# Kernel tuning notes

Hardware: AMD Instinct MI355X
Metric: run time of the kernel (lower is better)

## Reference

```python
import jax, jax.numpy as jnp
import numpy as np

L, D, H, F, E, K = 2, 512, 8, 2048, 8, 2
V, B, S, T, PAD = 32000, 2, 1024, 1024, 0


def _pe(n, d):
    pos = jnp.arange(n, dtype=jnp.float32)[:, None]
    div = jnp.exp(jnp.arange(0, d, 2, dtype=jnp.float32) * (-np.log(10000.0) / d))
    pe = jnp.zeros((n, d), jnp.float32)
    pe = pe.at[:, 0::2].set(jnp.sin(pos * div)).at[:, 1::2].set(jnp.cos(pos * div))
    return pe


def _ln(x, g, b):
    m = x.mean(-1, keepdims=True)
    v = ((x - m) ** 2).mean(-1, keepdims=True)
    return (x - m) / jnp.sqrt(v + 1e-5) * g + b


def _mha(q_in, k_in, v_in, w, b, mask):
    # w: [4,D,D] (q,k,v,out), b: [4,D]; mask broadcastable to [B,H,Sq,Sk] (True=keep)
    Bq, Sq, Dm = q_in.shape
    Sk = k_in.shape[1]
    dk = Dm // H
    q = (q_in @ w[0] + b[0]).reshape(Bq, Sq, H, dk).transpose(0, 2, 1, 3)
    k = (k_in @ w[1] + b[1]).reshape(Bq, Sk, H, dk).transpose(0, 2, 1, 3)
    v = (v_in @ w[2] + b[2]).reshape(Bq, Sk, H, dk).transpose(0, 2, 1, 3)
    s = jnp.einsum('bhqd,bhkd->bhqk', q, k) / np.sqrt(dk).astype(np.float32)
    s = jnp.where(mask, s, jnp.float32(-1e9))
    a = jax.nn.softmax(s, axis=-1)
    c = jnp.einsum('bhqk,bhkd->bhqd', a, v).transpose(0, 2, 1, 3).reshape(Bq, Sq, Dm)
    return c @ w[3] + b[3]


def _moe(x, gw, gb, w1, b1, w2, b2):
    # token-choice top-k routing with softmax gate probs (no renormalization)
    Bx, Sx, Dm = x.shape
    N = Bx * Sx
    xf = x.reshape(N, Dm)
    probs = jax.nn.softmax(xf @ gw + gb, axis=-1)              # [N,E]
    topv, topi = jax.lax.top_k(probs, K)                        # [N,K]
    comb = jnp.zeros_like(probs).at[jnp.arange(N)[:, None], topi].set(topv)  # [N,E] sparse combine weights
    h = jax.nn.relu(jnp.einsum('nd,edf->nef', xf, w1) + b1)     # [N,E,F]
    eo = jnp.einsum('nef,efd->ned', h, w2) + b2                 # [N,E,D]
    y = jnp.einsum('ne,ned->nd', comb, eo)
    return y.reshape(Bx, Sx, Dm)


def setup_inputs():
    key = jax.random.key(0)
    ks = iter(jax.random.split(key, 32))
    sd, sf = 1.0 / np.sqrt(D), 1.0 / np.sqrt(F)

    def nrm(shape, scale):
        return jax.random.normal(next(ks), shape, jnp.float32) * np.float32(scale)

    inp = {}
    inp['src'] = jax.random.randint(next(ks), (B, S), 0, V)
    inp['tgt'] = jax.random.randint(next(ks), (B, T), 0, V)
    inp['enc_emb'] = nrm((V, D), 0.02).at[PAD].set(0.0)
    inp['dec_emb'] = nrm((V, D), 0.02).at[PAD].set(0.0)
    inp['enc_attn_w'] = nrm((L, 4, D, D), sd)
    inp['enc_attn_b'] = jnp.zeros((L, 4, D), jnp.float32)
    inp['enc_ln_g'] = jnp.ones((L, 2, D), jnp.float32)
    inp['enc_ln_b'] = jnp.zeros((L, 2, D), jnp.float32)
    inp['enc_gate_w'] = nrm((L, D, E), sd)
    inp['enc_gate_b'] = jnp.zeros((L, E), jnp.float32)
    inp['enc_w1'] = nrm((L, E, D, F), sd)
    inp['enc_b1'] = jnp.zeros((L, E, F), jnp.float32)
    inp['enc_w2'] = nrm((L, E, F, D), sf)
    inp['enc_b2'] = jnp.zeros((L, E, D), jnp.float32)
    inp['dec_sa_w'] = nrm((L, 4, D, D), sd)
    inp['dec_sa_b'] = jnp.zeros((L, 4, D), jnp.float32)
    inp['dec_ca_w'] = nrm((L, 4, D, D), sd)
    inp['dec_ca_b'] = jnp.zeros((L, 4, D), jnp.float32)
    inp['dec_ln_g'] = jnp.ones((L, 3, D), jnp.float32)
    inp['dec_ln_b'] = jnp.zeros((L, 3, D), jnp.float32)
    inp['dec_gate_w'] = nrm((L, D, E), sd)
    inp['dec_gate_b'] = jnp.zeros((L, E), jnp.float32)
    inp['dec_w1'] = nrm((L, E, D, F), sd)
    inp['dec_b1'] = jnp.zeros((L, E, F), jnp.float32)
    inp['dec_w2'] = nrm((L, E, F, D), sf)
    inp['dec_b2'] = jnp.zeros((L, E, D), jnp.float32)
    inp['out_w'] = nrm((D, V), sd)
    inp['out_b'] = jnp.zeros((V,), jnp.float32)
    return inp


def reference(src, tgt, enc_emb, dec_emb, enc_attn_w, enc_attn_b, enc_ln_g, enc_ln_b,
              enc_gate_w, enc_gate_b, enc_w1, enc_b1, enc_w2, enc_b2,
              dec_sa_w, dec_sa_b, dec_ca_w, dec_ca_b, dec_ln_g, dec_ln_b,
              dec_gate_w, dec_gate_b, dec_w1, dec_b1, dec_w2, dec_b2, out_w, out_b):
    src_mask = (src != PAD)[:, None, None, :]                                  # [B,1,1,S]
    causal = jnp.tril(jnp.ones((T, T), bool))
    tgt_mask = (tgt != PAD)[:, None, None, :] & causal[None, None]             # [B,1,T,T]

    x = enc_emb[src] + _pe(S, D)[None]                                         # dropout = identity (eval)
    for l in range(L):
        a = _mha(x, x, x, enc_attn_w[l], enc_attn_b[l], src_mask)
        x = _ln(x + a, enc_ln_g[l, 0], enc_ln_b[l, 0])
        f = _moe(x, enc_gate_w[l], enc_gate_b[l], enc_w1[l], enc_b1[l], enc_w2[l], enc_b2[l])
        x = _ln(x + f, enc_ln_g[l, 1], enc_ln_b[l, 1])
    enc_out = x

    y = dec_emb[tgt] + _pe(T, D)[None]
    for l in range(L):
        a = _mha(y, y, y, dec_sa_w[l], dec_sa_b[l], tgt_mask)
        y = _ln(y + a, dec_ln_g[l, 0], dec_ln_b[l, 0])
        c = _mha(y, enc_out, enc_out, dec_ca_w[l], dec_ca_b[l], src_mask)
        y = _ln(y + c, dec_ln_g[l, 1], dec_ln_b[l, 1])
        f = _moe(y, dec_gate_w[l], dec_gate_b[l], dec_w1[l], dec_b1[l], dec_w2[l], dec_b2[l])
        y = _ln(y + f, dec_ln_g[l, 2], dec_ln_b[l, 2])

    return y @ out_w + out_b                                                    # [B,T,V]
```

## Files before the change

### kernel.cpp

```cpp
#include <hip/hip_runtime.h>
#include <hip/hip_bf16.h>

#define L_ 2
#define D_ 512
#define H_ 8
#define DK_ 64
#define F_ 2048
#define E_ 8
#define V_ 32000
#define B_ 2
#define S_ 1024
#define T_ 1024
#define NTOK (B_*S_)
#define MAXPAD 5120
#define RBLK   40
#define QLD 1536

typedef unsigned short u16;
typedef _Float16 f16x8 __attribute__((ext_vector_type(8)));
typedef _Float16 f16x4 __attribute__((ext_vector_type(4)));
typedef float f32x4 __attribute__((ext_vector_type(4)));

__device__ __forceinline__ void gload16(const void* g, const void* l) {
    __builtin_amdgcn_global_load_lds(
        (const __attribute__((address_space(1))) void*)g,
        (__attribute__((address_space(3))) void*)l, 16, 0, 0);
}

__device__ __forceinline__ void split_f16(float v, _Float16& h, _Float16& l) {
    h = (_Float16)v;
    l = (_Float16)(v - (float)h);
}

__global__ __launch_bounds__(256) void embed_pe(const int* __restrict__ toks,
                                                const float* __restrict__ emb,
                                                _Float16* __restrict__ oh,
                                                _Float16* __restrict__ ol, int Slen)
{
    int n = blockIdx.x;
    int spos = n % Slen;
    int tok = toks[n];
    const float* erow = emb + (size_t)tok * D_;
    size_t rb = (size_t)n * D_;
    for (int j = threadIdx.x; j < D_; j += 256) {
        int i = j >> 1;
        float arg = (float)spos * expf(-(float)i * 0.035977892f);
        float pe = (j & 1) ? cosf(arg) : sinf(arg);
        float v = erow[j] + pe;
        _Float16 h, l; split_f16(v, h, l);
        oh[rb + j] = h; ol[rb + j] = l;
    }
}

template<bool WLO>
__global__ __launch_bounds__(256) void transpose_w(const float* __restrict__ in,
                                                   _Float16* __restrict__ oh,
                                                   _Float16* __restrict__ ol, int R, int C)
{
    __shared__ float t[64][65];
    size_t sb = (size_t)blockIdx.z * R * C;
    in += sb; oh += sb; if (WLO) ol += sb;
    int c0 = blockIdx.x * 64, r0 = blockIdx.y * 64;
    int tid = threadIdx.x;
    {
        int r = tid >> 4;
        int cq = (tid & 15) * 4;
        #pragma unroll
        for (int p = 0; p < 4; ++p) {
            int rr = r + p * 16;
            float4 v = *(const float4*)&in[(size_t)(r0 + rr) * C + c0 + cq];
            t[rr][cq] = v.x; t[rr][cq + 1] = v.y; t[rr][cq + 2] = v.z; t[rr][cq + 3] = v.w;
        }
    }
    __syncthreads();
    int rp = (tid & 15) * 4;
    int cb = tid >> 4;
    #pragma unroll
    for (int p = 0; p < 4; ++p) {
        int c = cb + p * 16;
        f16x4 hv, lv;
        #pragma unroll
        for (int j = 0; j < 4; ++j) {
            float v = t[rp + j][c];
            _Float16 h = (_Float16)v;
            hv[j] = h;
            if (WLO) lv[j] = (_Float16)(v - (float)h);
        }
        *(f16x4*)&oh[(size_t)(c0 + c) * R + r0 + rp] = hv;
        if (WLO) *(f16x4*)&ol[(size_t)(c0 + c) * R + r0 + rp] = lv;
    }
}

__global__ __launch_bounds__(256) void transpose_w3(
    const float* __restrict__ i0, _Float16* __restrict__ h0, _Float16* __restrict__ l0,
    const float* __restrict__ i1, _Float16* __restrict__ h1, _Float16* __restrict__ l1,
    const float* __restrict__ i2, _Float16* __restrict__ h2, _Float16* __restrict__ l2)
{
    __shared__ float t[64][65];
    int set = blockIdx.z >> 3, sub = blockIdx.z & 7;
    const float* in = (set == 0) ? i0 : (set == 1) ? i1 : i2;
    _Float16* oh = (set == 0) ? h0 : (set == 1) ? h1 : h2;
    _Float16* ol = (set == 0) ? l0 : (set == 1) ? l1 : l2;
    size_t sb = (size_t)sub * D_ * D_;
    in += sb; oh += sb; ol += sb;
    int c0 = blockIdx.x * 64, r0 = blockIdx.y * 64;
    int tid = threadIdx.x;
    {
        int r = tid >> 4;
        int cq = (tid & 15) * 4;
        #pragma unroll
        for (int p = 0; p < 4; ++p) {
            int rr = r + p * 16;
            float4 v = *(const float4*)&in[(size_t)(r0 + rr) * D_ + c0 + cq];
            t[rr][cq] = v.x; t[rr][cq + 1] = v.y; t[rr][cq + 2] = v.z; t[rr][cq + 3] = v.w;
        }
    }
    __syncthreads();
    int rp = (tid & 15) * 4;
    int cb = tid >> 4;
    #pragma unroll
    for (int p = 0; p < 4; ++p) {
        int c = cb + p * 16;
        f16x4 hv, lv;
        #pragma unroll
        for (int j = 0; j < 4; ++j) {
            float v = t[rp + j][c];
            _Float16 h = (_Float16)v;
            hv[j] = h;
            lv[j] = (_Float16)(v - (float)h);
        }
        *(f16x4*)&oh[(size_t)(c0 + c) * D_ + r0 + rp] = hv;
        *(f16x4*)&ol[(size_t)(c0 + c) * D_ + r0 + rp] = lv;
    }
}

template<int MODE, bool RELU, int OUTMODE, int PASSES, int TM, int TN, bool SWZ>
__global__ __launch_bounds__(256, 2) void gemm_mfma(
    const _Float16* __restrict__ Ah, const _Float16* __restrict__ Al,
    const _Float16* __restrict__ Wh, const _Float16* __restrict__ Wl,
    const float* __restrict__ biasbase,
    float* __restrict__ Cf, _Float16* __restrict__ Ch, _Float16* __restrict__ Cl,
    _Float16* __restrict__ vt_h, _Float16* __restrict__ vt_l, int cbase,
    int M, int Kd, int N, int ldc,
    const int* __restrict__ route_tok, const int* __restrict__ rb_expert,
    const int* __restrict__ pad_base, const int* __restrict__ counts)
{
    constexpr int AR = TM / 32;
    constexpr int BR = TN / 32;
    int bx = blockIdx.x, by = blockIdx.y;
    if (SWZ) {
        int total = gridDim.x * gridDim.y;
        int n = by * gridDim.x + bx;
        int q = total >> 3;
        int w2 = (n & 7) * q + (n >> 3);
        bx = w2 % gridDim.x; by = w2 / gridDim.x;
    }
    int row0 = bx * TM;
    const _Float16* Wmh = Wh;
    const _Float16* Wml = Wl;
    const float* bias = biasbase;
    int vend = M;
    if (MODE != 0) {
        int total = pad_base[E_];
        if (row0 >= total) return;
        int e = rb_expert[row0 >> 7];
        vend = pad_base[e] + counts[e];
        Wmh = Wh + (size_t)e * Kd * N;
        if (PASSES == 3) Wml = Wl + (size_t)e * Kd * N;
        bias = biasbase + (size_t)e * N;
    }
    int col0 = by * TN;
    int tid = threadIdx.x;
    int lane = tid & 63, w = tid >> 6;
    int wm = w >> 1, wn = w & 1;

    __shared__ _Float16 lds[(PASSES == 3 ? 2 : 1) * (TM + TN) * 64];
    _Float16* lAh = lds;
    _Float16* lBh = lds + TM * 64;
    _Float16* lAl = (PASSES == 3) ? lds + (TM + TN) * 64 : nullptr;
    _Float16* lBl = (PASSES == 3) ? lds + (TM + TN) * 64 + TM * 64 : nullptr;

    int srow8 = lane >> 3;
    int q8 = lane & 7;
    size_t aoff[AR], boff[BR];
    #pragma unroll
    for (int j = 0; j < AR; ++j) {
        int m = w * (TM / 4) + j * 8 + srow8;
        int gr = row0 + m;
        int ar = (MODE == 1) ? route_tok[gr] : gr;
        int ss = (q8 ^ (m & 7)) << 3;
        aoff[j] = (size_t)ar * Kd + ss;
    }
    #pragma unroll
    for (int j = 0; j < BR; ++j) {
        int m = w * (TN / 4) + j * 8 + srow8;
        int ss = (q8 ^ (m & 7)) << 3;
        boff[j] = (size_t)(col0 + m) * Kd + ss;
    }

    f32x4 zero4 = {0.f, 0.f, 0.f, 0.f};
    f32x4 acc[AR][BR];
    #pragma unroll
    for (int i = 0; i < AR; ++i)
        #pragma unroll
        for (int j = 0; j < BR; ++j) acc[i][j] = zero4;

    int lm = lane & 15, kg = lane >> 4;

    for (int k0 = 0; k0 < Kd; k0 += 64) {
        #pragma unroll
        for (int j = 0; j < AR; ++j) {
            int lb = (w * (TM / 4) + j * 8) * 64;
            gload16(Ah + aoff[j] + k0, lAh + lb);
            if (PASSES == 3) gload16(Al + aoff[j] + k0, lAl + lb);
        }
        #pragma unroll
        for (int j = 0; j < BR; ++j) {
            int lb = (w * (TN / 4) + j * 8) * 64;
            gload16(Wmh + boff[j] + k0, lBh + lb);
            if (PASSES == 3) gload16(Wml + boff[j] + k0, lBl + lb);
        }
        __syncthreads();
        #pragma unroll
        for (int ks = 0; ks < 2; ++ks) {
            f16x8 ah[AR], bh[BR];
            #pragma unroll
            for (int i = 0; i < AR; ++i) {
                int m = wm * (TM / 2) + i * 16 + lm;
                ah[i] = *(const f16x8*)&lAh[m * 64 + ((((ks << 2) + kg) ^ (m & 7)) << 3)];
            }
            #pragma unroll
            for (int j = 0; j < BR; ++j) {
                int n = wn * (TN / 2) + j * 16 + lm;
                bh[j] = *(const f16x8*)&lBh[n * 64 + ((((ks << 2) + kg) ^ (n & 7)) << 3)];
            }
            #pragma unroll
            for (int i = 0; i < AR; ++i)
                #pragma unroll
                for (int jn = 0; jn < BR; ++jn)
                    acc[i][jn] = __builtin_amdgcn_mfma_f32_16x16x32_f16(ah[i], bh[jn], acc[i][jn], 0, 0, 0);
            if (PASSES == 3) {
                f16x8 bl[BR];
                #pragma unroll
                for (int j = 0; j < BR; ++j) {
                    int n = wn * (TN / 2) + j * 16 + lm;
                    bl[j] = *(const f16x8*)&lBl[n * 64 + ((((ks << 2) + kg) ^ (n & 7)) << 3)];
                }
                #pragma unroll
                for (int i = 0; i < AR; ++i)
                    #pragma unroll
                    for (int jn = 0; jn < BR; ++jn)
                        acc[i][jn] = __builtin_amdgcn_mfma_f32_16x16x32_f16(ah[i], bl[jn], acc[i][jn], 0, 0, 0);
                f16x8 al[AR];
                #pragma unroll
// ... 190 lines not shown
                    pv[jn][r] = p;
                    psum += p;
                }
                psum += __shfl_xor(psum, 1);
                psum += __shfl_xor(psum, 2);
                psum += __shfl_xor(psum, 4);
                psum += __shfl_xor(psum, 8);
                lreg[r] += psum;
                mreg[r] = mnew;
            }

            #pragma unroll
            for (int jn = 0; jn < 4; ++jn) {
                int col = jn * 16 + lm;
                #pragma unroll
                for (int r = 0; r < 4; ++r) {
                    int rr = (lane >> 4) * 4 + r;
                    int idx = rr * 64 + (((col >> 3) ^ (rr & 7)) << 3) + (col & 7);
                    _Float16 hh, ll; split_f16(pv[jn][r], hh, ll);
                    lPh[idx] = hh; lPl[idx] = ll;
                }
            }

            #pragma unroll
            for (int ks = 0; ks < 2; ++ks) {
                int poff = lm * 64 + ((((ks << 2) + kg) ^ (lm & 7)) << 3);
                f16x8 pah = *(const f16x8*)&lPh[poff];
                f16x8 pal = *(const f16x8*)&lPl[poff];
                #pragma unroll
                for (int jn = 0; jn < 4; ++jn) {
                    int n = jn * 16 + lm;
                    int noff = n * 64 + ((((ks << 2) + kg) ^ (n & 7)) << 3);
                    f16x8 vbh = *(const f16x8*)&lVh[noff];
                    f16x8 vbl = *(const f16x8*)&lVl[noff];
                    od[jn] = __builtin_amdgcn_mfma_f32_16x16x32_f16(pah, vbh, od[jn], 0, 0, 0);
                    od[jn] = __builtin_amdgcn_mfma_f32_16x16x32_f16(pah, vbl, od[jn], 0, 0, 0);
                    od[jn] = __builtin_amdgcn_mfma_f32_16x16x32_f16(pal, vbh, od[jn], 0, 0, 0);
                }
            }
        }
        __syncthreads();
    }

    float* mrg = (float*)(smem + 32768);
    if (kh == 1) {
        float* mp = mrg + ((size_t)qg * 64 + lane) * 24;
        #pragma unroll
        for (int jn = 0; jn < 4; ++jn)
            #pragma unroll
            for (int r = 0; r < 4; ++r) mp[jn * 4 + r] = od[jn][r];
        #pragma unroll
        for (int r = 0; r < 4; ++r) { mp[16 + r] = mreg[r]; mp[20 + r] = lreg[r]; }
    }
    __syncthreads();
    if (kh == 0) {
        float* mp = mrg + ((size_t)qg * 64 + lane) * 24;
        #pragma unroll
        for (int r = 0; r < 4; ++r) {
            float m1 = mp[16 + r], l1 = mp[20 + r];
            float m = fmaxf(mreg[r], m1);
            float c0 = expf(mreg[r] - m), c1 = expf(m1 - m);
            float inv = 1.0f / (lreg[r] * c0 + l1 * c1);
            size_t rbase = (size_t)(tb + qrow[r]) * D_ + h * DK_;
            #pragma unroll
            for (int jn = 0; jn < 4; ++jn) {
                float o = (od[jn][r] * c0 + mp[jn * 4 + r] * c1) * inv;
                _Float16 hh, ll; split_f16(o, hh, ll);
                int d = jn * 16 + lm;
                ch[rbase + d] = hh; cl[rbase + d] = ll;
            }
        }
    }
}

template<bool GATE>
__global__ __launch_bounds__(256) void ln_add(const _Float16* __restrict__ xh,
                                              const _Float16* __restrict__ xl,
                                              const float* __restrict__ r,
                                              const float* __restrict__ g,
                                              const float* __restrict__ be,
                                              _Float16* __restrict__ oh,
                                              _Float16* __restrict__ ol,
                                              const float* __restrict__ gw,
                                              const float* __restrict__ gb,
                                              float* __restrict__ lg)
{
    int row = blockIdx.x;
    size_t rb = (size_t)row * D_;
    int tid = threadIdx.x;
    float v0 = (float)xh[rb + tid] + (float)xl[rb + tid] + r[rb + tid];
    float v1 = (float)xh[rb + tid + 256] + (float)xl[rb + tid + 256] + r[rb + tid + 256];
    float s = v0 + v1;
    for (int off = 32; off; off >>= 1) s += __shfl_down(s, off);
    __shared__ float red[8];
    __shared__ float gred[4][E_];
    int lane = tid & 63, wid = tid >> 6;
    if (!lane) red[wid] = s;
    __syncthreads();
    if (!tid) red[4] = (red[0] + red[1] + red[2] + red[3]) * (1.0f / 512.0f);
    __syncthreads();
    float m = red[4];
    float d0 = v0 - m, d1 = v1 - m;
    s = d0 * d0 + d1 * d1;
    for (int off = 32; off; off >>= 1) s += __shfl_down(s, off);
    if (!lane) red[wid] = s;
    __syncthreads();
    if (!tid) red[5] = rsqrtf((red[0] + red[1] + red[2] + red[3]) * (1.0f / 512.0f) + 1e-5f);
    __syncthreads();
    float rstd = red[5];
    float y0 = d0 * rstd * g[tid] + be[tid];
    float y1 = d1 * rstd * g[tid + 256] + be[tid + 256];
    _Float16 h, l;
    split_f16(y0, h, l); oh[rb + tid] = h; ol[rb + tid] = l;
    split_f16(y1, h, l); oh[rb + tid + 256] = h; ol[rb + tid + 256] = l;
    if (GATE) {
        float acc[E_];
        const float* g0 = gw + (size_t)tid * E_;
        const float* g1 = gw + (size_t)(tid + 256) * E_;
        #pragma unroll
        for (int e = 0; e < E_; ++e) acc[e] = y0 * g0[e] + y1 * g1[e];
        #pragma unroll
        for (int e = 0; e < E_; ++e)
            for (int off = 32; off; off >>= 1) acc[e] += __shfl_down(acc[e], off);
        if (!lane) {
            #pragma unroll
            for (int e = 0; e < E_; ++e) gred[wid][e] = acc[e];
        }
        __syncthreads();
        if (tid < E_)
            lg[(size_t)row * E_ + tid] = gred[0][tid] + gred[1][tid] + gred[2][tid] + gred[3][tid] + gb[tid];
    }
}

__global__ __launch_bounds__(256) void ln_add_moe(const _Float16* __restrict__ xh,
                                                  const _Float16* __restrict__ xl,
                                                  const float* __restrict__ eo,
                                                  const float* __restrict__ topv,
                                                  const int* __restrict__ route_row,
                                                  const float* __restrict__ g,
                                                  const float* __restrict__ be,
                                                  _Float16* __restrict__ oh,
                                                  _Float16* __restrict__ ol)
{
    int row = blockIdx.x;
    int r0 = route_row[row * 2], r1 = route_row[row * 2 + 1];
    float w0 = topv[row * 2], w1 = topv[row * 2 + 1];
    size_t rb = (size_t)row * D_;
    const float* e0 = eo + (size_t)r0 * D_;
    const float* e1 = eo + (size_t)r1 * D_;
    int tid = threadIdx.x;
    float v0 = (float)xh[rb + tid] + (float)xl[rb + tid] + w0 * e0[tid] + w1 * e1[tid];
    float v1 = (float)xh[rb + tid + 256] + (float)xl[rb + tid + 256] + w0 * e0[tid + 256] + w1 * e1[tid + 256];
    float s = v0 + v1;
    for (int off = 32; off; off >>= 1) s += __shfl_down(s, off);
    __shared__ float red[8];
    int lane = tid & 63, wid = tid >> 6;
    if (!lane) red[wid] = s;
    __syncthreads();
    if (!tid) red[4] = (red[0] + red[1] + red[2] + red[3]) * (1.0f / 512.0f);
    __syncthreads();
    float m = red[4];
    float d0 = v0 - m, d1 = v1 - m;
    s = d0 * d0 + d1 * d1;
    for (int off = 32; off; off >>= 1) s += __shfl_down(s, off);
    if (!lane) red[wid] = s;
    __syncthreads();
    if (!tid) red[5] = rsqrtf((red[0] + red[1] + red[2] + red[3]) * (1.0f / 512.0f) + 1e-5f);
    __syncthreads();
    float rstd = red[5];
    float y0 = d0 * rstd * g[tid] + be[tid];
    float y1 = d1 * rstd * g[tid + 256] + be[tid + 256];
    _Float16 h, l;
    split_f16(y0, h, l); oh[rb + tid] = h; ol[rb + tid] = l;
    split_f16(y1, h, l); oh[rb + tid + 256] = h; ol[rb + tid + 256] = l;
}

__global__ __launch_bounds__(1024) void gate_top2_routes(const float* __restrict__ lg,
                                                         float* __restrict__ topv,
                                                         int* __restrict__ route_tok,
                                                         int* __restrict__ route_row,
                                                         int* __restrict__ counts,
                                                         int* __restrict__ pad_base,
                                                         int* __restrict__ rb_expert)
{
    __shared__ int eid[NTOK * 2];
    __shared__ unsigned short chist[256][8];
    __shared__ unsigned short segb[8][16];
    __shared__ int pb[E_ + 1];
    __shared__ int cnt[E_];
    int t = threadIdx.x;
    #pragma unroll
    for (int s2 = 0; s2 < 2; ++s2) {
        int n = t * 2 + s2;
        float l0[E_], p[E_];
        float m = -1e30f;
        #pragma unroll
        for (int e = 0; e < E_; ++e) { l0[e] = lg[n * E_ + e]; m = fmaxf(m, l0[e]); }
        float su = 0.f;
        #pragma unroll
        for (int e = 0; e < E_; ++e) { p[e] = expf(l0[e] - m); su += p[e]; }
        float inv = 1.0f / su;
        int i1 = 0; float v1 = p[0];
        #pragma unroll
        for (int e = 1; e < E_; ++e) if (p[e] > v1) { v1 = p[e]; i1 = e; }
        int i2 = -1; float v2 = -1.f;
        #pragma unroll
        for (int e = 0; e < E_; ++e) if (e != i1 && p[e] > v2) { v2 = p[e]; i2 = e; }
        topv[n * 2] = v1 * inv; topv[n * 2 + 1] = v2 * inv;
        eid[n * 2] = i1; eid[n * 2 + 1] = i2;
    }
    #pragma unroll
    for (int g = 0; g < 5; ++g) route_tok[t + 1024 * g] = 0;
    __syncthreads();

    if (t < 256) {
        int r[16];
        #pragma unroll
        for (int i = 0; i < 16; ++i) r[i] = eid[t * 16 + i];
        #pragma unroll
        for (int e = 0; e < 8; ++e) {
            int h = 0;
            #pragma unroll
            for (int i = 0; i < 16; ++i) h += (r[i] == e) ? 1 : 0;
            chist[t][e] = (unsigned short)h;
        }
    }
    __syncthreads();

    if (t < 128) {
        int e = t >> 4, seg = t & 15;
        int s = 0;
        #pragma unroll
        for (int i = 0; i < 16; ++i) s += chist[seg * 16 + i][e];
        segb[e][seg] = (unsigned short)s;
    }
    __syncthreads();
    if (t < 8) {
        int run = 0;
        #pragma unroll
        for (int sg = 0; sg < 16; ++sg) {
            int v = segb[t][sg];
            segb[t][sg] = (unsigned short)run;
            run += v;
        }
        cnt[t] = run;
        counts[t] = run;
    }
    __syncthreads();
    if (t < 128) {
        int e = t >> 4, seg = t & 15;
        int run = segb[e][seg];
        #pragma unroll
        for (int i = 0; i < 16; ++i) {
            int c = seg * 16 + i;
            int v = chist[c][e];
            chist[c][e] = (unsigned short)run;
            run += v;
        }
    }
    __syncthreads();

    if (t == 0) {
        int pad = 0;
        for (int e = 0; e < 8; ++e) {
            pb[e] = pad;
            pad_base[e] = pad;
            int nb = (cnt[e] + 127) >> 7;
            for (int rb = 0; rb < nb; ++rb) rb_expert[(pad >> 7) + rb] = e;
            pad += nb << 7;
        }
        pb[8] = pad;
        pad_base[8] = pad;
    }
    __syncthreads();

    if (t < 256) {
        int r[16];
        #pragma unroll
        for (int i = 0; i < 16; ++i) r[i] = eid[t * 16 + i];
        #pragma unroll
        for (int e = 0; e < 8; ++e) {
            int o = pb[e] + chist[t][e];
            #pragma unroll
            for (int i = 0; i < 16; ++i) {
                if (r[i] == e) {
                    int slot = t * 16 + i;
                    route_tok[o] = slot >> 1;
                    route_row[slot] = o;
                    o++;
                }
            }
        }
    }
}

extern "C" void kernel_launch(void* const* d_in, const int* in_sizes, int n_in,
                              void* d_out, int out_size, void* d_ws, size_t ws_size,
                              hipStream_t stream)
{
    const int*   src        = (const int*)  d_in[0];
    const int*   tgt        = (const int*)  d_in[1];
    const float* enc_emb    = (const float*)d_in[2];
    const float* dec_emb    = (const float*)d_in[3];
    const float* enc_attn_w = (const float*)d_in[4];
    const float* enc_attn_b = (const float*)d_in[5];
    const float* enc_ln_g   = (const float*)d_in[6];
    const float* enc_ln_b   = (const float*)d_in[7];
    const float* enc_gate_w = (const float*)d_in[8];
    const float* enc_gate_b = (const float*)d_in[9];
    const float* enc_w1     = (const float*)d_in[10];
    const float* enc_b1     = (const float*)d_in[11];
    const float* enc_w2     = (const float*)d_in[12];
    const float* enc_b2     = (const float*)d_in[13];
    const float* dec_sa_w   = (const float*)d_in[14];
    const float* dec_sa_b   = (const float*)d_in[15];
    const float* dec_ca_w   = (const float*)d_in[16];
    const float* dec_ca_b   = (const float*)d_in[17];
    const float* dec_ln_g   = (const float*)d_in[18];
    const float* dec_ln_b   = (const float*)d_in[19];
    const float* dec_gate_w = (const float*)d_in[20];
    const float* dec_gate_b = (const float*)d_in[21];
    const float* dec_w1     = (const float*)d_in[22];
    const float* dec_b1     = (const float*)d_in[23];
    const float* dec_w2     = (const float*)d_in[24];
    const float* dec_b2     = (const float*)d_in[25];
    const float* out_w      = (const float*)d_in[26];
    const float* out_b      = (const float*)d_in[27];
    float* out = (float*)d_out;

    char* ob = (char*)d_out;
    size_t oc = 0;
    auto dalloc = [&](size_t bytes) { char* p = ob + oc; oc += (bytes + 255) & ~(size_t)255; return p; };
    _Float16* qkv_h  = (_Float16*)dalloc((size_t)NTOK * QLD * 2);
    _Float16* qkv_l  = (_Float16*)dalloc((size_t)NTOK * QLD * 2);
    _Float16* vt_h   = (_Float16*)dalloc((size_t)16 * 64 * 1024 * 2);
    _Float16* vt_l   = (_Float16*)dalloc((size_t)16 * 64 * 1024 * 2);
    float* aout  = (float*)dalloc((size_t)NTOK * D_ * 4);
    _Float16* ctx_h = (_Float16*)dalloc((size_t)NTOK * D_ * 2);
    _Float16* ctx_l = (_Float16*)dalloc((size_t)NTOK * D_ * 2);
    _Float16* encA_h = (_Float16*)dalloc((size_t)L_ * 4 * D_ * D_ * 2);
    _Float16* encA_l = (_Float16*)dalloc((size_t)L_ * 4 * D_ * D_ * 2);
    _Float16* saA_h  = (_Float16*)dalloc((size_t)L_ * 4 * D_ * D_ * 2);
    _Float16* saA_l  = (_Float16*)dalloc((size_t)L_ * 4 * D_ * D_ * 2);
    _Float16* caA_h  = (_Float16*)dalloc((size_t)L_ * 4 * D_ * D_ * 2);
    _Float16* caA_l  = (_Float16*)dalloc((size_t)L_ * 4 * D_ * D_ * 2);
    _Float16* xA_h = (_Float16*)dalloc((size_t)NTOK * D_ * 2);
    _Float16* xA_l = (_Float16*)dalloc((size_t)NTOK * D_ * 2);
    _Float16* xB_h = (_Float16*)dalloc((size_t)NTOK * D_ * 2);
    _Float16* xB_l = (_Float16*)dalloc((size_t)NTOK * D_ * 2);
    _Float16* yA_h = (_Float16*)dalloc((size_t)NTOK * D_ * 2);
    _Float16* yA_l = (_Float16*)dalloc((size_t)NTOK * D_ * 2);
    _Float16* yB_h = (_Float16*)dalloc((size_t)NTOK * D_ * 2);
    _Float16* yB_l = (_Float16*)dalloc((size_t)NTOK * D_ * 2);

    char* wp = (char*)d_ws;
    size_t wc = 0;
    auto walloc = [&](size_t bytes) { char* p = wp + wc; wc += (bytes + 255) & ~(size_t)255; return p; };
    _Float16* outwT_h = (_Float16*)walloc((size_t)V_ * D_ * 2);
    _Float16* final_h = (_Float16*)walloc((size_t)NTOK * D_ * 2);
    size_t wsz = (size_t)L_ * E_ * D_ * F_;
    _Float16* ew1t_h = (_Float16*)walloc(wsz * 2);
    _Float16* ew1t_l = (_Float16*)walloc(wsz * 2);
    _Float16* ew2t_h = (_Float16*)walloc(wsz * 2);
    _Float16* ew2t_l = (_Float16*)walloc(wsz * 2);
    _Float16* dw1t_h = (_Float16*)walloc(wsz * 2);
    _Float16* dw1t_l = (_Float16*)walloc(wsz * 2);
    _Float16* dw2t_h = (_Float16*)walloc(wsz * 2);
    _Float16* dw2t_l = (_Float16*)walloc(wsz * 2);
    _Float16* hbuf_h  = (_Float16*)walloc((size_t)MAXPAD * F_ * 2);
    _Float16* hbuf_l  = (_Float16*)walloc((size_t)MAXPAD * F_ * 2);
    float*    eobuf   = (float*)walloc((size_t)MAXPAD * D_ * 4);
    float* lg   = (float*)walloc((size_t)NTOK * E_ * 4);
    float* topv = (float*)walloc((size_t)NTOK * 2 * 4);
    int*   route_tok = (int*)walloc((size_t)MAXPAD * 4);
    int*   route_row = (int*)walloc((size_t)NTOK * 2 * 4);
    int*   counts    = (int*)walloc(64);
    int*   pad_base  = (int*)walloc(64);
    int*   rb_expert = (int*)walloc((size_t)128 * 4);

    transpose_w3<<<dim3(8, 8, 24), 256, 0, stream>>>(
        enc_attn_w, encA_h, encA_l, dec_sa_w, saA_h, saA_l, dec_ca_w, caA_h, caA_l);
    transpose_w<false><<<dim3(500, 8, 1), 256, 0, stream>>>(out_w, outwT_h, nullptr, D_, V_);
    transpose_w<true><<<dim3(32, 8, L_ * E_), 256, 0, stream>>>(enc_w1, ew1t_h, ew1t_l, D_, F_);
    transpose_w<true><<<dim3(8, 32, L_ * E_), 256, 0, stream>>>(enc_w2, ew2t_h, ew2t_l, F_, D_);
    transpose_w<true><<<dim3(32, 8, L_ * E_), 256, 0, stream>>>(dec_w1, dw1t_h, dw1t_l, D_, F_);
    transpose_w<true><<<dim3(8, 32, L_ * E_), 256, 0, stream>>>(dec_w2, dw2t_h, dw2t_l, F_, D_);

    auto run_mha = [&](const _Float16* q_h, const _Float16* q_l,
                       const _Float16* kv_h, const _Float16* kv_l,
                       const _Float16* wT_h, const _Float16* wT_l, const float* bt,
                       const int* ktoks, int causal, bool fused) {
        if (fused) {
            gemm_mfma<0, false, 2, 3, 64, 128, false><<<dim3(32, 12), 256, 0, stream>>>(
                q_h, q_l, wT_h, wT_l, bt, nullptr, qkv_h, qkv_l, vt_h, vt_l, 0,
                NTOK, D_, 1536, QLD, nullptr, nullptr, nullptr, nullptr);
        } else {
            gemm_mfma<0, false, 1, 3, 64, 64, false><<<dim3(32, 8), 256, 0, stream>>>(
                q_h, q_l, wT_h, wT_l, bt, nullptr, qkv_h, qkv_l, nullptr, nullptr, 0,
                NTOK, D_, 512, QLD, nullptr, nullptr, nullptr, nullptr);
            gemm_mfma<0, false, 2, 3, 64, 128, false><<<dim3(32, 8), 256, 0, stream>>>(
                kv_h, kv_l, wT_h + (size_t)D_ * D_, wT_l + (size_t)D_ * D_, bt + D_,
                nullptr, qkv_h, qkv_l, vt_h, vt_l, 512,
                NTOK, D_, 1024, QLD, nullptr, nullptr, nullptr, nullptr);
        }
        if (causal)
            attn_flash<1><<<dim3(16, 16), 512, 0, stream>>>(qkv_h, qkv_l, vt_h, vt_l, ktoks, ctx_h, ctx_l);
        else
            attn_flash<0><<<dim3(16, 16), 512, 0, stream>>>(qkv_h, qkv_l, vt_h, vt_l, ktoks, ctx_h, ctx_l);
        gemm_mfma<0, false, 0, 3, 64, 64, false><<<dim3(32, 8), 256, 0, stream>>>(
            ctx_h, ctx_l, wT_h + (size_t)3 * D_ * D_, wT_l + (size_t)3 * D_ * D_,
            bt + 3 * D_, aout, nullptr, nullptr, nullptr, nullptr, 0,
            NTOK, D_, 512, 512, nullptr, nullptr, nullptr, nullptr);
    };

    auto run_moe = [&](const _Float16* x_h, const _Float16* x_l,
                       const _Float16* w1h, const _Float16* w1l,
                       const _Float16* w2h, const _Float16* w2l,
                       const float* b1p, const float* b2p, bool p3) {
        gate_top2_routes<<<1, 1024, 0, stream>>>(lg, topv, route_tok, route_row, counts, pad_base, rb_expert);
        if (p3) {
            gemm_mfma<1, true, 1, 3, 128, 128, false><<<dim3(RBLK, 16), 256, 0, stream>>>(
                x_h, x_l, w1h, w1l, b1p, nullptr, hbuf_h, hbuf_l, nullptr, nullptr, 0,
                0, D_, F_, F_, route_tok, rb_expert, pad_base, counts);
            gemm_mfma<2, false, 0, 3, 128, 64, false><<<dim3(RBLK, 8), 256, 0, stream>>>(
                hbuf_h, hbuf_l, w2h, w2l, b2p, eobuf, nullptr, nullptr, nullptr, nullptr, 0,
                0, F_, D_, D_, route_tok, rb_expert, pad_base, counts);
        } else {
            gemm_mfma<1, true, 1, 1, 128, 128, false><<<dim3(RBLK, 16), 256, 0, stream>>>(
                x_h, nullptr, w1h, nullptr, b1p, nullptr, hbuf_h, hbuf_l, nullptr, nullptr, 0,
                0, D_, F_, F_, route_tok, rb_expert, pad_base, counts);
            gemm_mfma<2, false, 0, 1, 128, 64, false><<<dim3(RBLK, 8), 256, 0, stream>>>(
                hbuf_h, nullptr, w2h, nullptr, b2p, eobuf, nullptr, nullptr, nullptr, nullptr, 0,
                0, F_, D_, D_, route_tok, rb_expert, pad_base, counts);
        }
    };

    embed_pe<<<B_ * S_, 256, 0, stream>>>(src, enc_emb, xA_h, xA_l, S_);
    _Float16* cur_h = xA_h; _Float16* cur_l = xA_l;
    _Float16* alt_h = xB_h; _Float16* alt_l = xB_l;
    for (int l = 0; l < L_; ++l) {
        run_mha(cur_h, cur_l, nullptr, nullptr,
                encA_h + (size_t)l * 4 * D_ * D_, encA_l + (size_t)l * 4 * D_ * D_,
                enc_attn_b + (size_t)l * 4 * D_, src, 0, true);
        ln_add<true><<<NTOK, 256, 0, stream>>>(cur_h, cur_l, aout,
            enc_ln_g + (size_t)(l * 2 + 0) * D_, enc_ln_b + (size_t)(l * 2 + 0) * D_,
            alt_h, alt_l, enc_gate_w + (size_t)l * D_ * E_, enc_gate_b + (size_t)l * E_, lg);
        { _Float16* t = cur_h; cur_h = alt_h; alt_h = t; t = cur_l; cur_l = alt_l; alt_l = t; }
        run_moe(cur_h, cur_l,
                ew1t_h + (size_t)l * E_ * D_ * F_, ew1t_l + (size_t)l * E_ * D_ * F_,
                ew2t_h + (size_t)l * E_ * D_ * F_, ew2t_l + (size_t)l * E_ * D_ * F_,
                enc_b1 + (size_t)l * E_ * F_, enc_b2 + (size_t)l * E_ * D_, true);
        ln_add_moe<<<NTOK, 256, 0, stream>>>(cur_h, cur_l, eobuf, topv, route_row,
            enc_ln_g + (size_t)(l * 2 + 1) * D_, enc_ln_b + (size_t)(l * 2 + 1) * D_,
            alt_h, alt_l);
        { _Float16* t = cur_h; cur_h = alt_h; alt_h = t; t = cur_l; cur_l = alt_l; alt_l = t; }
    }
    _Float16* enc_h = cur_h; _Float16* enc_l = cur_l;

    embed_pe<<<B_ * T_, 256, 0, stream>>>(tgt, dec_emb, yA_h, yA_l, T_);
    _Float16* dc_h = yA_h; _Float16* dc_l = yA_l;
    _Float16* da_h = yB_h; _Float16* da_l = yB_l;
    for (int l = 0; l < L_; ++l) {
        run_mha(dc_h, dc_l, nullptr, nullptr,
                saA_h + (size_t)l * 4 * D_ * D_, saA_l + (size_t)l * 4 * D_ * D_,
                dec_sa_b + (size_t)l * 4 * D_, tgt, 1, true);
        ln_add<false><<<NTOK, 256, 0, stream>>>(dc_h, dc_l, aout,
            dec_ln_g + (size_t)(l * 3 + 0) * D_, dec_ln_b + (size_t)(l * 3 + 0) * D_,
            da_h, da_l, nullptr, nullptr, nullptr);
        { _Float16* t = dc_h; dc_h = da_h; da_h = t; t = dc_l; dc_l = da_l; da_l = t; }
        run_mha(dc_h, dc_l, enc_h, enc_l,
                caA_h + (size_t)l * 4 * D_ * D_, caA_l + (size_t)l * 4 * D_ * D_,
                dec_ca_b + (size_t)l * 4 * D_, src, 0, false);
        ln_add<true><<<NTOK, 256, 0, stream>>>(dc_h, dc_l, aout,
            dec_ln_g + (size_t)(l * 3 + 1) * D_, dec_ln_b + (size_t)(l * 3 + 1) * D_,
            da_h, da_l, dec_gate_w + (size_t)l * D_ * E_, dec_gate_b + (size_t)l * E_, lg);
        { _Float16* t = dc_h; dc_h = da_h; da_h = t; t = dc_l; dc_l = da_l; da_l = t; }
        bool last = (l == L_ - 1);
        run_moe(dc_h, dc_l,
                dw1t_h + (size_t)l * E_ * D_ * F_, dw1t_l + (size_t)l * E_ * D_ * F_,
                dw2t_h + (size_t)l * E_ * D_ * F_, dw2t_l + (size_t)l * E_ * D_ * F_,
                dec_b1 + (size_t)l * E_ * F_, dec_b2 + (size_t)l * E_ * D_, !last);
        ln_add_moe<<<NTOK, 256, 0, stream>>>(dc_h, dc_l, eobuf, topv, route_row,
            dec_ln_g + (size_t)(l * 3 + 2) * D_, dec_ln_b + (size_t)(l * 3 + 2) * D_,
            last ? final_h : da_h, da_l);
        { _Float16* t = dc_h; dc_h = da_h; da_h = t; t = dc_l; dc_l = da_l; da_l = t; }
    }

    gemm_mfma<0, false, 0, 1, 128, 128, true><<<dim3(NTOK / 128, V_ / 128), 256, 0, stream>>>(
        final_h, nullptr, outwT_h, nullptr, out_b, out, nullptr, nullptr, nullptr, nullptr, 0,
        NTOK, D_, V_, V_, nullptr, nullptr, nullptr, nullptr);
}
```

Before: 1.251 ms.

## Use 64-row MoE tiles, warp-per-row layernorm, and drop output GEMM swizzle

Expert blocks are now padded to 64 rows instead of 128, and the MoE GEMMs use 64-row tiles, which cuts wasted padded rows and launches more blocks. The layernorm kernels (plain, gated and MoE-combine) now handle one row per wavefront with 8-wide vector loads and xor-shuffle reductions, removing shared-memory barriers. The blockIdx swizzle on the vocabulary projection GEMM is removed, which may change L2 reuse of the output weights. Smaller tiles reduce reuse per block inside the MoE GEMMs.

```diff
diff --git a/kernel.cpp b/kernel.cpp
--- a/kernel.cpp
+++ b/kernel.cpp
@@ -12,8 +12,8 @@
 #define S_ 1024
 #define T_ 1024
 #define NTOK (B_*S_)
-#define MAXPAD 5120
-#define RBLK   40
+#define MAXPAD 4608
+#define RB64   72
 #define QLD 1536
 
 typedef unsigned short u16;
@@ -134,7 +134,7 @@
     }
 }
 
-template<int MODE, bool RELU, int OUTMODE, int PASSES, int TM, int TN, bool SWZ>
+template<int MODE, bool RELU, int OUTMODE, int PASSES, int TM, int TN>
 __global__ __launch_bounds__(256, 2) void gemm_mfma(
     const _Float16* __restrict__ Ah, const _Float16* __restrict__ Al,
     const _Float16* __restrict__ Wh, const _Float16* __restrict__ Wl,
@@ -147,15 +147,7 @@
 {
     constexpr int AR = TM / 32;
     constexpr int BR = TN / 32;
-    int bx = blockIdx.x, by = blockIdx.y;
-    if (SWZ) {
-        int total = gridDim.x * gridDim.y;
-        int n = by * gridDim.x + bx;
-        int q = total >> 3;
-        int w2 = (n & 7) * q + (n >> 3);
-        bx = w2 % gridDim.x; by = w2 / gridDim.x;
-    }
-    int row0 = bx * TM;
+    int row0 = blockIdx.x * TM;
     const _Float16* Wmh = Wh;
     const _Float16* Wml = Wl;
     const float* bias = biasbase;
@@ -163,13 +155,13 @@
     if (MODE != 0) {
         int total = pad_base[E_];
         if (row0 >= total) return;
-        int e = rb_expert[row0 >> 7];
+        int e = rb_expert[row0 >> 6];
         vend = pad_base[e] + counts[e];
         Wmh = Wh + (size_t)e * Kd * N;
         if (PASSES == 3) Wml = Wl + (size_t)e * Kd * N;
         bias = biasbase + (size_t)e * N;
     }
-    int col0 = by * TN;
+    int col0 = blockIdx.y * TN;
     int tid = threadIdx.x;
     int lane = tid & 63, w = tid >> 6;
     int wm = w >> 1, wn = w & 1;
@@ -526,53 +518,76 @@
                                               _Float16* __restrict__ oh,
                                               _Float16* __restrict__ ol,
                                               const float* __restrict__ gw,
-                                              const float* __restrict__ gb,
+                                              const float* __restrict__ gbias,
                                               float* __restrict__ lg)
 {
-    int row = blockIdx.x;
-    size_t rb = (size_t)row * D_;
-    int tid = threadIdx.x;
-    float v0 = (float)xh[rb + tid] + (float)xl[rb + tid] + r[rb + tid];
-    float v1 = (float)xh[rb + tid + 256] + (float)xl[rb + tid + 256] + r[rb + tid + 256];
-    float s = v0 + v1;
-    for (int off = 32; off; off >>= 1) s += __shfl_down(s, off);
-    __shared__ float red[8];
-    __shared__ float gred[4][E_];
-    int lane = tid & 63, wid = tid >> 6;
-    if (!lane) red[wid] = s;
-    __syncthreads();
-    if (!tid) red[4] = (red[0] + red[1] + red[2] + red[3]) * (1.0f / 512.0f);
-    __syncthreads();
-    float m = red[4];
-    float d0 = v0 - m, d1 = v1 - m;
-    s = d0 * d0 + d1 * d1;
-    for (int off = 32; off; off >>= 1) s += __shfl_down(s, off);
-    if (!lane) red[wid] = s;
-    __syncthreads();
-    if (!tid) red[5] = rsqrtf((red[0] + red[1] + red[2] + red[3]) * (1.0f / 512.0f) + 1e-5f);
-    __syncthreads();
-    float rstd = red[5];
-    float y0 = d0 * rstd * g[tid] + be[tid];
-    float y1 = d1 * rstd * g[tid + 256] + be[tid + 256];
-    _Float16 h, l;
-    split_f16(y0, h, l); oh[rb + tid] = h; ol[rb + tid] = l;
-    split_f16(y1, h, l); oh[rb + tid + 256] = h; ol[rb + tid + 256] = l;
+    int w = threadIdx.x >> 6, lane = threadIdx.x & 63;
+    int row = blockIdx.x * 4 + w;
+    int col = lane * 8;
+    size_t rb = (size_t)row * D_ + col;
+    f16x8 vh = *(const f16x8*)&xh[rb];
+    f16x8 vl = *(const f16x8*)&xl[rb];
+    float4 ra = *(const float4*)&r[rb];
+    float4 rc = *(const float4*)&r[rb + 4];
+    float v[8];
+    v[0] = (float)vh[0] + (float)vl[0] + ra.x;
+    v[1] = (float)vh[1] + (float)vl[1] + ra.y;
+    v[2] = (float)vh[2] + (float)vl[2] + ra.z;
+    v[3] = (float)vh[3] + (float)vl[3] + ra.w;
+    v[4] = (float)vh[4] + (float)vl[4] + rc.x;
+    v[5] = (float)vh[5] + (float)vl[5] + rc.y;
+    v[6] = (float)vh[6] + (float)vl[6] + rc.z;
+    v[7] = (float)vh[7] + (float)vl[7] + rc.w;
+    float s = 0.f;
+    #pragma unroll
+    for (int i = 0; i < 8; ++i) s += v[i];
+    #pragma unroll
+    for (int off = 32; off; off >>= 1) s += __shfl_xor(s, off);
+    float m = s * (1.0f / 512.0f);
+    float d[8];
+    float q = 0.f;
+    #pragma unroll
+    for (int i = 0; i < 8; ++i) { d[i] = v[i] - m; q += d[i] * d[i]; }
+    #pragma unroll
+    for (int off = 32; off; off >>= 1) q += __shfl_xor(q, off);
+    float rstd = rsqrtf(q * (1.0f / 512.0f) + 1e-5f);
+    float4 ga = *(const float4*)&g[col];
+    float4 gc = *(const float4*)&g[col + 4];
+    float4 ba = *(const float4*)&be[col];
+    float4 bc = *(const float4*)&be[col + 4];
+    float gg[8] = {ga.x, ga.y, ga.z, ga.w, gc.x, gc.y, gc.z, gc.w};
+    float bb[8] = {ba.x, ba.y, ba.z, ba.w, bc.x, bc.y, bc.z, bc.w};
+    float y[8];
+    f16x8 ohv, olv;
+    #pragma unroll
+    for (int i = 0; i < 8; ++i) {
+        y[i] = d[i] * rstd * gg[i] + bb[i];
+        _Float16 h2, l2; split_f16(y[i], h2, l2);
+        ohv[i] = h2; olv[i] = l2;
+    }
+    *(f16x8*)&oh[rb] = ohv;
+    *(f16x8*)&ol[rb] = olv;
     if (GATE) {
-        float acc[E_];
-        const float* g0 = gw + (size_t)tid * E_;
-        const float* g1 = gw + (size_t)(tid + 256) * E_;
-        #pragma unroll
-        for (int e = 0; e < E_; ++e) acc[e] = y0 * g0[e] + y1 * g1[e];
+        float acc[E_] = {0.f, 0.f, 0.f, 0.f, 0.f, 0.f, 0.f, 0.f};
+        #pragma unroll
+        for (int i = 0; i < 8; ++i) {
+            const float* gp = gw + (size_t)(col + i) * E_;
+            float4 g0 = *(const float4*)gp;
+            float4 g1 = *(const float4*)(gp + 4);
+            acc[0] += y[i] * g0.x; acc[1] += y[i] * g0.y;
+            acc[2] += y[i] * g0.z; acc[3] += y[i] * g0.w;
+            acc[4] += y[i] * g1.x; acc[5] += y[i] * g1.y;
+            acc[6] += y[i] * g1.z; acc[7] += y[i] * g1.w;
+        }
         #pragma unroll
         for (int e = 0; e < E_; ++e)
-            for (int off = 32; off; off >>= 1) acc[e] += __shfl_down(acc[e], off);
-        if (!lane) {
-            #pragma unroll
-            for (int e = 0; e < E_; ++e) gred[wid][e] = acc[e];
-        }
-        __syncthreads();
-        if (tid < E_)
-            lg[(size_t)row * E_ + tid] = gred[0][tid] + gred[1][tid] + gred[2][tid] + gred[3][tid] + gb[tid];
+            #pragma unroll
+            for (int off = 32; off; off >>= 1) acc[e] += __shfl_xor(acc[e], off);
+        if (lane == 0) {
+            float* lp = lg + (size_t)row * E_;
+            #pragma unroll
+            for (int e = 0; e < E_; ++e) lp[e] = acc[e] + gbias[e];
+        }
     }
 }
 
@@ -586,37 +601,57 @@
                                                   _Float16* __restrict__ oh,
                                                   _Float16* __restrict__ ol)
 {
-    int row = blockIdx.x;
+    int w = threadIdx.x >> 6, lane = threadIdx.x & 63;
+    int row = blockIdx.x * 4 + w;
     int r0 = route_row[row * 2], r1 = route_row[row * 2 + 1];
     float w0 = topv[row * 2], w1 = topv[row * 2 + 1];
-    size_t rb = (size_t)row * D_;
-    const float* e0 = eo + (size_t)r0 * D_;
-    const float* e1 = eo + (size_t)r1 * D_;
-    int tid = threadIdx.x;
-    float v0 = (float)xh[rb + tid] + (float)xl[rb + tid] + w0 * e0[tid] + w1 * e1[tid];
-    float v1 = (float)xh[rb + tid + 256] + (float)xl[rb + tid + 256] + w0 * e0[tid + 256] + w1 * e1[tid + 256];
-    float s = v0 + v1;
-    for (int off = 32; off; off >>= 1) s += __shfl_down(s, off);
-    __shared__ float red[8];
-    int lane = tid & 63, wid = tid >> 6;
-    if (!lane) red[wid] = s;
-    __syncthreads();
-    if (!tid) red[4] = (red[0] + red[1] + red[2] + red[3]) * (1.0f / 512.0f);
-    __syncthreads();
-    float m = red[4];
-    float d0 = v0 - m, d1 = v1 - m;
-    s = d0 * d0 + d1 * d1;
-    for (int off = 32; off; off >>= 1) s += __shfl_down(s, off);
-    if (!lane) red[wid] = s;
-    __syncthreads();
-    if (!tid) red[5] = rsqrtf((red[0] + red[1] + red[2] + red[3]) * (1.0f / 512.0f) + 1e-5f);
-    __syncthreads();
-    float rstd = red[5];
-    float y0 = d0 * rstd * g[tid] + be[tid];
-    float y1 = d1 * rstd * g[tid + 256] + be[tid + 256];
-    _Float16 h, l;
-    split_f16(y0, h, l); oh[rb + tid] = h; ol[rb + tid] = l;
-    split_f16(y1, h, l); oh[rb + tid + 256] = h; ol[rb + tid + 256] = l;
+    int col = lane * 8;
+    size_t rb = (size_t)row * D_ + col;
+    f16x8 vh = *(const f16x8*)&xh[rb];
+    f16x8 vl = *(const f16x8*)&xl[rb];
+    const float* e0 = eo + (size_t)r0 * D_ + col;
+    const float* e1 = eo + (size_t)r1 * D_ + col;
+    float4 e0a = *(const float4*)e0;
+    float4 e0b = *(const float4*)(e0 + 4);
+    float4 e1a = *(const float4*)e1;
+    float4 e1b = *(const float4*)(e1 + 4);
+    float v[8];
+    v[0] = (float)vh[0] + (float)vl[0] + w0 * e0a.x + w1 * e1a.x;
+    v[1] = (float)vh[1] + (float)vl[1] + w0 * e0a.y + w1 * e1a.y;
+    v[2] = (float)vh[2] + (float)vl[2] + w0 * e0a.z + w1 * e1a.z;
+    v[3] = (float)vh[3] + (float)vl[3] + w0 * e0a.w + w1 * e1a.w;
+    v[4] = (float)vh[4] + (float)vl[4] + w0 * e0b.x + w1 * e1b.x;
+    v[5] = (float)vh[5] + (float)vl[5] + w0 * e0b.y + w1 * e1b.y;
+    v[6] = (float)vh[6] + (float)vl[6] + w0 * e0b.z + w1 * e1b.z;
+    v[7] = (float)vh[7] + (float)vl[7] + w0 * e0b.w + w1 * e1b.w;
+    float s = 0.f;
+    #pragma unroll
+    for (int i = 0; i < 8; ++i) s += v[i];
+    #pragma unroll
+    for (int off = 32; off; off >>= 1) s += __shfl_xor(s, off);
+    float m = s * (1.0f / 512.0f);
+    float d[8];
+    float q = 0.f;
+    #pragma unroll
+    for (int i = 0; i < 8; ++i) { d[i] = v[i] - m; q += d[i] * d[i]; }
+    #pragma unroll
+    for (int off = 32; off; off >>= 1) q += __shfl_xor(q, off);
+    float rstd = rsqrtf(q * (1.0f / 512.0f) + 1e-5f);
+    float4 ga = *(const float4*)&g[col];
+    float4 gc = *(const float4*)&g[col + 4];
+    float4 ba = *(const float4*)&be[col];
+    float4 bc = *(const float4*)&be[col + 4];
+    float gg[8] = {ga.x, ga.y, ga.z, ga.w, gc.x, gc.y, gc.z, gc.w};
+    float bb[8] = {ba.x, ba.y, ba.z, ba.w, bc.x, bc.y, bc.z, bc.w};
+    f16x8 ohv, olv;
+    #pragma unroll
+    for (int i = 0; i < 8; ++i) {
+        float y = d[i] * rstd * gg[i] + bb[i];
+        _Float16 h2, l2; split_f16(y, h2, l2);
+        ohv[i] = h2; olv[i] = l2;
+    }
+    *(f16x8*)&oh[rb] = ohv;
+    *(f16x8*)&ol[rb] = olv;
 }
 
 __global__ __launch_bounds__(1024) void gate_top2_routes(const float* __restrict__ lg,
@@ -709,9 +744,9 @@
         for (int e = 0; e < 8; ++e) {
             pb[e] = pad;
             pad_base[e] = pad;
-            int nb = (cnt[e] + 127) >> 7;
-            for (int rb = 0; rb < nb; ++rb) rb_expert[(pad >> 7) + rb] = e;
-            pad += nb << 7;
+            int nb = (cnt[e] + 63) >> 6;
+            for (int rb = 0; rb < nb; ++rb) rb_expert[(pad >> 6) + rb] = e;
+            pad += nb << 6;
         }
         pb[8] = pad;
         pad_base[8] = pad;
@@ -811,12 +846,12 @@
     _Float16* dw1t_l = (_Float16*)walloc(wsz * 2);
     _Float16* dw2t_h = (_Float16*)walloc(wsz * 2);
     _Float16* dw2t_l = (_Float16*)walloc(wsz * 2);
-    _Float16* hbuf_h  = (_Float16*)walloc((size_t)MAXPAD * F_ * 2);
-    _Float16* hbuf_l  = (_Float16*)walloc((size_t)MAXPAD * F_ * 2);
-    float*    eobuf   = (float*)walloc((size_t)MAXPAD * D_ * 4);
+    _Float16* hbuf_h  = (_Float16*)walloc((size_t)5120 * F_ * 2);
+    _Float16* hbuf_l  = (_Float16*)walloc((size_t)5120 * F_ * 2);
+    float*    eobuf   = (float*)walloc((size_t)5120 * D_ * 4);
     float* lg   = (float*)walloc((size_t)NTOK * E_ * 4);
     float* topv = (float*)walloc((size_t)NTOK * 2 * 4);
-    int*   route_tok = (int*)walloc((size_t)MAXPAD * 4);
+    int*   route_tok = (int*)walloc((size_t)5120 * 4);
     int*   route_row = (int*)walloc((size_t)NTOK * 2 * 4);
     int*   counts    = (int*)walloc(64);
     int*   pad_base  = (int*)walloc(64);
@@ -835,14 +870,14 @@
                        const _Float16* wT_h, const _Float16* wT_l, const float* bt,
                        const int* ktoks, int causal, bool fused) {
         if (fused) {
-            gemm_mfma<0, false, 2, 3, 64, 128, false><<<dim3(32, 12), 256, 0, stream>>>(
+            gemm_mfma<0, false, 2, 3, 64, 128><<<dim3(32, 12), 256, 0, stream>>>(
                 q_h, q_l, wT_h, wT_l, bt, nullptr, qkv_h, qkv_l, vt_h, vt_l, 0,
                 NTOK, D_, 1536, QLD, nullptr, nullptr, nullptr, nullptr);
         } else {
-            gemm_mfma<0, false, 1, 3, 64, 64, false><<<dim3(32, 8), 256, 0, stream>>>(
+            gemm_mfma<0, false, 1, 3, 64, 64><<<dim3(32, 8), 256, 0, stream>>>(
                 q_h, q_l, wT_h, wT_l, bt, nullptr, qkv_h, qkv_l, nullptr, nullptr, 0,
                 NTOK, D_, 512, QLD, nullptr, nullptr, nullptr, nullptr);
-            gemm_mfma<0, false, 2, 3, 64, 128, false><<<dim3(32, 8), 256, 0, stream>>>(
+            gemm_mfma<0, false, 2, 3, 64, 128><<<dim3(32, 8), 256, 0, stream>>>(
                 kv_h, kv_l, wT_h + (size_t)D_ * D_, wT_l + (size_t)D_ * D_, bt + D_,
                 nullptr, qkv_h, qkv_l, vt_h, vt_l, 512,
                 NTOK, D_, 1024, QLD, nullptr, nullptr, nullptr, nullptr);
@@ -851,7 +886,7 @@
             attn_flash<1><<<dim3(16, 16), 512, 0, stream>>>(qkv_h, qkv_l, vt_h, vt_l, ktoks, ctx_h, ctx_l);
         else
             attn_flash<0><<<dim3(16, 16), 512, 0, stream>>>(qkv_h, qkv_l, vt_h, vt_l, ktoks, ctx_h, ctx_l);
-        gemm_mfma<0, false, 0, 3, 64, 64, false><<<dim3(32, 8), 256, 0, stream>>>(
+        gemm_mfma<0, false, 0, 3, 64, 64><<<dim3(32, 8), 256, 0, stream>>>(
             ctx_h, ctx_l, wT_h + (size_t)3 * D_ * D_, wT_l + (size_t)3 * D_ * D_,
             bt + 3 * D_, aout, nullptr, nullptr, nullptr, nullptr, 0,
             NTOK, D_, 512, 512, nullptr, nullptr, nullptr, nullptr);
@@ -863,17 +898,17 @@
                        const float* b1p, const float* b2p, bool p3) {
         gate_top2_routes<<<1, 1024, 0, stream>>>(lg, topv, route_tok, route_row, counts, pad_base, rb_expert);
         if (p3) {
-            gemm_mfma<1, true, 1, 3, 128, 128, false><<<dim3(RBLK, 16), 256, 0, stream>>>(
+            gemm_mfma<1, true, 1, 3, 64, 128><<<dim3(RB64, 16), 256, 0, stream>>>(
                 x_h, x_l, w1h, w1l, b1p, nullptr, hbuf_h, hbuf_l, nullptr, nullptr, 0,
                 0, D_, F_, F_, route_tok, rb_expert, pad_base, counts);
-            gemm_mfma<2, false, 0, 3, 128, 64, false><<<dim3(RBLK, 8), 256, 0, stream>>>(
+            gemm_mfma<2, false, 0, 3, 64, 64><<<dim3(RB64, 8), 256, 0, stream>>>(
                 hbuf_h, hbuf_l, w2h, w2l, b2p, eobuf, nullptr, nullptr, nullptr, nullptr, 0,
                 0, F_, D_, D_, route_tok, rb_expert, pad_base, counts);
         } else {
-            gemm_mfma<1, true, 1, 1, 128, 128, false><<<dim3(RBLK, 16), 256, 0, stream>>>(
+            gemm_mfma<1, true, 1, 1, 64, 128><<<dim3(RB64, 16), 256, 0, stream>>>(
                 x_h, nullptr, w1h, nullptr, b1p, nullptr, hbuf_h, hbuf_l, nullptr, nullptr, 0,
                 0, D_, F_, F_, route_tok, rb_expert, pad_base, counts);
-            gemm_mfma<2, false, 0, 1, 128, 64, false><<<dim3(RBLK, 8), 256, 0, stream>>>(
+            gemm_mfma<2, false, 0, 1, 64, 64><<<dim3(RB64, 8), 256, 0, stream>>>(
                 hbuf_h, nullptr, w2h, nullptr, b2p, eobuf, nullptr, nullptr, nullptr, nullptr, 0,
                 0, F_, D_, D_, route_tok, rb_expert, pad_base, counts);
         }
@@ -886,7 +921,7 @@
         run_mha(cur_h, cur_l, nullptr, nullptr,
                 encA_h + (size_t)l * 4 * D_ * D_, encA_l + (size_t)l * 4 * D_ * D_,
                 enc_attn_b + (size_t)l * 4 * D_, src, 0, true);
-        ln_add<true><<<NTOK, 256, 0, stream>>>(cur_h, cur_l, aout,
+        ln_add<true><<<NTOK / 4, 256, 0, stream>>>(cur_h, cur_l, aout,
             enc_ln_g + (size_t)(l * 2 + 0) * D_, enc_ln_b + (size_t)(l * 2 + 0) * D_,
             alt_h, alt_l, enc_gate_w + (size_t)l * D_ * E_, enc_gate_b + (size_t)l * E_, lg);
         { _Float16* t = cur_h; cur_h = alt_h; alt_h = t; t = cur_l; cur_l = alt_l; alt_l = t; }
@@ -894,7 +929,7 @@
                 ew1t_h + (size_t)l * E_ * D_ * F_, ew1t_l + (size_t)l * E_ * D_ * F_,
                 ew2t_h + (size_t)l * E_ * D_ * F_, ew2t_l + (size_t)l * E_ * D_ * F_,
                 enc_b1 + (size_t)l * E_ * F_, enc_b2 + (size_t)l * E_ * D_, true);
-        ln_add_moe<<<NTOK, 256, 0, stream>>>(cur_h, cur_l, eobuf, topv, route_row,
+        ln_add_moe<<<NTOK / 4, 256, 0, stream>>>(cur_h, cur_l, eobuf, topv, route_row,
             enc_ln_g + (size_t)(l * 2 + 1) * D_, enc_ln_b + (size_t)(l * 2 + 1) * D_,
             alt_h, alt_l);
         { _Float16* t = cur_h; cur_h = alt_h; alt_h = t; t = cur_l; cur_l = alt_l; alt_l = t; }
@@ -908,14 +943,14 @@
         run_mha(dc_h, dc_l, nullptr, nullptr,
                 saA_h + (size_t)l * 4 * D_ * D_, saA_l + (size_t)l * 4 * D_ * D_,
                 dec_sa_b + (size_t)l * 4 * D_, tgt, 1, true);
-        ln_add<false><<<NTOK, 256, 0, stream>>>(dc_h, dc_l, aout,
+        ln_add<false><<<NTOK / 4, 256, 0, stream>>>(dc_h, dc_l, aout,
             dec_ln_g + (size_t)(l * 3 + 0) * D_, dec_ln_b + (size_t)(l * 3 + 0) * D_,
             da_h, da_l, nullptr, nullptr, nullptr);
         { _Float16* t = dc_h; dc_h = da_h; da_h = t; t = dc_l; dc_l = da_l; da_l = t; }
         run_mha(dc_h, dc_l, enc_h, enc_l,
                 caA_h + (size_t)l * 4 * D_ * D_, caA_l + (size_t)l * 4 * D_ * D_,
                 dec_ca_b + (size_t)l * 4 * D_, src, 0, false);
-        ln_add<true><<<NTOK, 256, 0, stream>>>(dc_h, dc_l, aout,
+        ln_add<true><<<NTOK / 4, 256, 0, stream>>>(dc_h, dc_l, aout,
             dec_ln_g + (size_t)(l * 3 + 1) * D_, dec_ln_b + (size_t)(l * 3 + 1) * D_,
             da_h, da_l, dec_gate_w + (size_t)l * D_ * E_, dec_gate_b + (size_t)l * E_, lg);
         { _Float16* t = dc_h; dc_h = da_h; da_h = t; t = dc_l; dc_l = da_l; da_l = t; }
@@ -924,13 +959,13 @@
                 dw1t_h + (size_t)l * E_ * D_ * F_, dw1t_l + (size_t)l * E_ * D_ * F_,
                 dw2t_h + (size_t)l * E_ * D_ * F_, dw2t_l + (size_t)l * E_ * D_ * F_,
                 dec_b1 + (size_t)l * E_ * F_, dec_b2 + (size_t)l * E_ * D_, !last);
-        ln_add_moe<<<NTOK, 256, 0, stream>>>(dc_h, dc_l, eobuf, topv, route_row,
+        ln_add_moe<<<NTOK / 4, 256, 0, stream>>>(dc_h, dc_l, eobuf, topv, route_row,
             dec_ln_g + (size_t)(l * 3 + 2) * D_, dec_ln_b + (size_t)(l * 3 + 2) * D_,
             last ? final_h : da_h, da_l);
         { _Float16* t = dc_h; dc_h = da_h; da_h = t; t = dc_l; dc_l = da_l; da_l = t; }
     }
 
-    gemm_mfma<0, false, 0, 1, 128, 128, true><<<dim3(NTOK / 128, V_ / 128), 256, 0, stream>>>(
+    gemm_mfma<0, false, 0, 1, 128, 128><<<dim3(NTOK / 128, V_ / 128), 256, 0, stream>>>(
         final_h, nullptr, outwT_h, nullptr, out_b, out, nullptr, nullptr, nullptr, nullptr, 0,
         NTOK, D_, V_, V_, nullptr, nullptr, nullptr, nullptr);
 }
```

Result: faster. 1.199 ms (median of 2 runs) (-4.2%).
